# Optimization experiments

Measured on AMD Instinct MI355X. Metric: run time of the kernel, lower is better.

The kernel has to match this reference:

```python
import jax, jax.numpy as jnp
import numpy as np

N = 50000
E = 800000
IN = 256
HID = 64
HEADS = 4
EPS = 1e-5


def batchnorm(x, g, b):
    # training-mode BatchNorm1d over node dim, biased variance (torch semantics)
    mu = jnp.mean(x, axis=0)
    var = jnp.mean((x - mu) ** 2, axis=0)
    return (x - mu) * jax.lax.rsqrt(var + EPS) * g + b


def gat(x, edge_index, W, a_src, a_dst, bias, heads, out_ch, num_nodes):
    src, dst = edge_index[0], edge_index[1]
    h = (x @ W).reshape(num_nodes, heads, out_ch)          # [N,H,C]
    al_s = jnp.einsum('nhc,hc->nh', h, a_src)              # [N,H]
    al_d = jnp.einsum('nhc,hc->nh', h, a_dst)
    e = jax.nn.leaky_relu(al_s[src] + al_d[dst], 0.2)      # [E,H]
    # segment softmax over destination neighborhoods
    m = jax.ops.segment_max(e, dst, num_segments=num_nodes)
    m = jnp.where(jnp.isfinite(m), m, 0.0)
    ex = jnp.exp(e - m[dst])                               # [E,H]
    denom = jax.ops.segment_sum(ex, dst, num_segments=num_nodes)
    alpha = ex / (denom[dst] + 1e-16)                      # [E,H]
    msg = alpha[:, :, None] * h[src]                       # [E,H,C]
    out = jax.ops.segment_sum(msg, dst, num_segments=num_nodes)
    return out.reshape(num_nodes, heads * out_ch) + bias


def setup_inputs() -> dict:
    key = jax.random.key(0)
    ks = jax.random.split(key, 12)
    d = {}
    d['x'] = jax.random.normal(ks[0], (N, IN), jnp.float32)
    d['edge_index'] = jax.random.randint(ks[1], (2, E), 0, N, jnp.int32)
    d['bn1_g'] = jnp.ones((IN,), jnp.float32)
    d['bn1_b'] = jnp.zeros((IN,), jnp.float32)
    d['lin1_W'] = jax.random.normal(ks[2], (IN, HID * HEADS), jnp.float32) * (1.0 / np.sqrt(IN))
    d['lin1_b'] = jnp.zeros((HID * HEADS,), jnp.float32)
    d['con1_W'] = jax.random.normal(ks[3], (IN, HID * HEADS), jnp.float32) * (1.0 / np.sqrt(IN))
    d['con1_asrc'] = jax.random.normal(ks[4], (HEADS, HID), jnp.float32) * 0.1
    d['con1_adst'] = jax.random.normal(ks[5], (HEADS, HID), jnp.float32) * 0.1
    d['con1_b'] = jnp.zeros((HID * HEADS,), jnp.float32)
    d['bn3_g'] = jnp.ones((HID * HEADS,), jnp.float32)
    d['bn3_b'] = jnp.zeros((HID * HEADS,), jnp.float32)
    d['lin3_W'] = jax.random.normal(ks[6], (HID * HEADS, 2), jnp.float32) * (1.0 / np.sqrt(HID * HEADS))
    d['lin3_b'] = jnp.zeros((2,), jnp.float32)
    d['con3_W'] = jax.random.normal(ks[7], (HID * HEADS, 2), jnp.float32) * (1.0 / np.sqrt(HID * HEADS))
    d['con3_asrc'] = jax.random.normal(ks[8], (1, 2), jnp.float32) * 0.1
    d['con3_adst'] = jax.random.normal(ks[9], (1, 2), jnp.float32) * 0.1
    d['con3_b'] = jnp.zeros((2,), jnp.float32)
    return d


def reference(x, edge_index, bn1_g, bn1_b, lin1_W, lin1_b, con1_W, con1_asrc, con1_adst, con1_b,
              bn3_g, bn3_b, lin3_W, lin3_b, con3_W, con3_asrc, con3_adst, con3_b):
    x = batchnorm(x, bn1_g, bn1_b)
    x = jax.nn.relu(x @ lin1_W + lin1_b
                    + gat(x, edge_index, con1_W, con1_asrc, con1_adst, con1_b, HEADS, HID, N))
    x = batchnorm(x, bn3_g, bn3_b)
    x = jax.nn.relu(x @ lin3_W + lin3_b
                    + gat(x, edge_index, con3_W, con3_asrc, con3_adst, con3_b, 1, 2, N))
    return x
```

## Files before the change

kernel.cpp:

```cpp
#include <hip/hip_runtime.h>
#include <math.h>

#define NN 50000
#define NE 800000
#define IC 256
#define EPS 1e-5f
#define P8 50176

typedef __attribute__((ext_vector_type(8))) short short8;
typedef __attribute__((ext_vector_type(4))) float f32x4;

enum : int {
  OFF_S1     = 0,
  OFF_S2     = 256,
  OFF_BAR    = 512,
  OFF_C8     = 528,
  ZERO_END   = OFF_C8 + 8 * P8,
  OFF_COFF   = ZERO_END,
  OFF_START  = OFF_COFF + 8 * P8,
  OFF_RANK   = OFF_START + 50004,
  OFF_BSM    = OFF_RANK + 200000,
  OFF_ALS    = OFF_BSM + 1024,
  OFF_ALD    = OFF_ALS + 200000,
  OFF_SRCS   = OFF_ALD + 200000,
  OFF_Y32    = OFF_SRCS + 800000,
  OFF_ND4    = OFF_Y32 + 100000,
  OFF_BFH    = OFF_ND4 + 200000,
  OFF_HBF    = OFF_BFH + 65536,
  OFF_YLBF   = OFF_HBF + 6400000,
  WS_FLOATS  = OFF_YLBF + 6400000
};

__device__ __forceinline__ float lrelu(float s) { return s > 0.f ? s : 0.2f * s; }
__device__ __forceinline__ float b2f(unsigned short u) {
  return __uint_as_float(((unsigned)u) << 16);
}
__device__ __forceinline__ unsigned short f2bf(float f) {
  unsigned u = __float_as_uint(f);
  return (unsigned short)((u + 0x7fffu + ((u >> 16) & 1u)) >> 16);
}
__device__ __forceinline__ unsigned cvtpk(float lo, float hi) {
  unsigned r;
  asm("v_cvt_pk_bf16_f32 %0, %1, %2" : "=v"(r) : "v"(lo), "v"(hi));
  return r;
}

__global__ __launch_bounds__(256) void k_prep(const float* __restrict__ x,
                                              float* __restrict__ S1,
                                              float* __restrict__ S2,
                                              const float* __restrict__ Wlin,
                                              const float* __restrict__ Wcon,
                                              unsigned short* __restrict__ Bfh) {
  int b = blockIdx.x;
  if (b < 1024) {
    int c = threadIdx.x;
    float s1 = 0.f, s2 = 0.f;
    for (int r0 = b * 8; r0 < NN; r0 += 8192) {
#pragma unroll
      for (int u = 0; u < 8; ++u) {
        int r = r0 + u;
        if (r < NN) {
          float v = x[r * IC + c];
          s1 += v;
          s2 = fmaf(v, v, s2);
        }
      }
    }
    atomicAdd(&S1[c], s1);
    atomicAdd(&S2[c], s2);
  } else {
    int id = (b - 1024) * 256 + threadIdx.x;
    int j = id & 7, lane = (id >> 3) & 63, nt = (id >> 9) & 31, ks = id >> 14;
    int k = ks * 32 + ((lane >> 4) << 3) + j;
    int n = nt * 16 + (lane & 15);
    float v = (n < 256) ? Wlin[k * 256 + n] : Wcon[k * 256 + (n - 256)];
    Bfh[id] = f2bf(v);
  }
}

__global__ __launch_bounds__(256) void k_bnstats2(const ushort4* __restrict__ x1q,
                                                  float* __restrict__ S1,
                                                  float* __restrict__ S2) {
  __shared__ float red1[4][256], red2[4][256];
  const int tid = threadIdx.x, wave = tid >> 6, lane = tid & 63;
  float s1a = 0.f, s1b = 0.f, s1c = 0.f, s1d = 0.f;
  float s2a = 0.f, s2b = 0.f, s2c = 0.f, s2d = 0.f;
  for (int r = blockIdx.x * 4 + wave; r < NN; r += gridDim.x * 4) {
    ushort4 v = x1q[r * 64 + lane];
    float f0 = b2f(v.x), f1 = b2f(v.y), f2 = b2f(v.z), f3 = b2f(v.w);
    s1a += f0; s2a = fmaf(f0, f0, s2a);
    s1b += f1; s2b = fmaf(f1, f1, s2b);
    s1c += f2; s2c = fmaf(f2, f2, s2c);
    s1d += f3; s2d = fmaf(f3, f3, s2d);
  }
  red1[wave][lane * 4 + 0] = s1a; red2[wave][lane * 4 + 0] = s2a;
  red1[wave][lane * 4 + 1] = s1b; red2[wave][lane * 4 + 1] = s2b;
  red1[wave][lane * 4 + 2] = s1c; red2[wave][lane * 4 + 2] = s2c;
  red1[wave][lane * 4 + 3] = s1d; red2[wave][lane * 4 + 3] = s2d;
  __syncthreads();
  float a = red1[0][tid] + red1[1][tid] + red1[2][tid] + red1[3][tid];
  float b = red2[0][tid] + red2[1][tid] + red2[2][tid] + red2[3][tid];
  atomicAdd(&S1[tid], a);
  atomicAdd(&S2[tid], b);
}

__global__ __launch_bounds__(256, 4) void k_gemm(const float* __restrict__ x,
                                                 const float* __restrict__ S1,
                                                 const float* __restrict__ S2,
                                                 const float* __restrict__ bng,
                                                 const float* __restrict__ bnb,
                                                 const unsigned short* __restrict__ Bfh,
                                                 unsigned short* __restrict__ ylbf,
                                                 unsigned short* __restrict__ hbf,
                                                 const float* __restrict__ asrc,
                                                 const float* __restrict__ adst,
                                                 float* __restrict__ als,
                                                 float* __restrict__ ald,
                                                 const int* __restrict__ dst,
                                                 int* __restrict__ counts8,
                                                 unsigned char* __restrict__ rank8) {
  const int tid = threadIdx.x;
  const int g = blockIdx.x;
  if (g >= 1568) {
    int hb = g - 1568;
    int e = hb * 256 + tid;
    int copy = hb & 7;
    int old = atomicAdd(&counts8[copy * P8 + dst[e]], 1);
    rank8[e] = (unsigned char)old;
    return;
  }
  const int row_blk = (g >> 4) * 8 + (g & 7);
  const int bn = (g >> 3) & 1;
  if (row_blk >= 782) return;
  const int row0 = row_blk * 64;
  __shared__ unsigned short Ah[2048];
  __shared__ float sc[256], sh[256];
  const int wave = tid >> 6, lane = tid & 63;
  {
    float mu = S1[tid] * (1.f / NN);
    float var = S2[tid] * (1.f / NN) - mu * mu;
    float ss = bng[tid] / sqrtf(var + EPS);
    sc[tid] = ss;
    sh[tid] = bnb[tid] - mu * ss;
  }
  const float4* x4 = (const float4*)x;
  const short8* Bh8 = (const short8*)Bfh;
  f32x4 acc[4][4];
#pragma unroll
  for (int i = 0; i < 4; ++i)
#pragma unroll
    for (int j = 0; j < 4; ++j) acc[i][j] = (f32x4){0.f, 0.f, 0.f, 0.f};

  const int m = tid >> 2, kg = tid & 3;
  const int r = row0 + m;
  const int aaddr = (((m >> 4) * 64) + ((m & 15) | (kg << 4))) * 8;
  __syncthreads();

  for (int ks = 0; ks < 8; ++ks) {
    const int c0 = ks * 32 + kg * 8;
    float v[8];
    if (r < NN) {
      int base = (r * IC + c0) >> 2;
      float4 fa = x4[base], fb = x4[base + 1];
      v[0] = fa.x; v[1] = fa.y; v[2] = fa.z; v[3] = fa.w;
      v[4] = fb.x; v[5] = fb.y; v[6] = fb.z; v[7] = fb.w;
#pragma unroll
      for (int j = 0; j < 8; ++j) v[j] = fmaf(v[j], sc[c0 + j], sh[c0 + j]);
    } else {
#pragma unroll
      for (int j = 0; j < 8; ++j) v[j] = 0.f;
    }
    unsigned ph[4];
#pragma unroll
    for (int j = 0; j < 4; ++j) ph[j] = cvtpk(v[2 * j], v[2 * j + 1]);
    *(uint4*)&Ah[aaddr] = make_uint4(ph[0], ph[1], ph[2], ph[3]);
    __syncthreads();

    short8 ah[4];
#pragma unroll
    for (int mt = 0; mt < 4; ++mt)
      ah[mt] = *(const short8*)&Ah[(mt * 64 + lane) * 8];
#pragma unroll
    for (int nt = 0; nt < 4; ++nt) {
      short8 bh = Bh8[(ks * 32 + bn * 16 + wave * 4 + nt) * 64 + lane];
#pragma unroll
      for (int mt = 0; mt < 4; ++mt)
        acc[mt][nt] = __builtin_amdgcn_mfma_f32_16x16x32_bf16(ah[mt], bh, acc[mt][nt], 0, 0, 0);
    }
    __syncthreads();
  }
  const int colq = lane & 15, quad = lane >> 4;
  if (bn == 0) {
#pragma unroll
    for (int mt = 0; mt < 4; ++mt)
#pragma unroll
      for (int reg = 0; reg < 4; ++reg) {
        int rr = row0 + mt * 16 + quad * 4 + reg;
        if (rr < NN) {
#pragma unroll
          for (int nt = 0; nt < 4; ++nt)
            ylbf[rr * IC + wave * 64 + nt * 16 + colq] = f2bf(acc[mt][nt][reg]);
        }
      }
  } else {
    const int head = wave;
    float asv[4], adv[4];
#pragma unroll
    for (int j = 0; j < 4; ++j) {
      asv[j] = asrc[head * 64 + j * 16 + colq];
      adv[j] = adst[head * 64 + j * 16 + colq];
    }
#pragma unroll
    for (int mt = 0; mt < 4; ++mt)
#pragma unroll
      for (int reg = 0; reg < 4; ++reg) {
        int rr = row0 + mt * 16 + quad * 4 + reg;
        float sA = 0.f, dA = 0.f;
#pragma unroll
        for (int j = 0; j < 4; ++j) {
          float hA = acc[mt][j][reg];
          sA = fmaf(hA, asv[j], sA);
          dA = fmaf(hA, adv[j], dA);
          if (rr < NN) hbf[rr * IC + head * 64 + j * 16 + colq] = f2bf(hA);
        }
#pragma unroll
        for (int off = 1; off < 16; off <<= 1) {
          sA += __shfl_xor(sA, off, 64);
          dA += __shfl_xor(dA, off, 64);
        }
        if (rr < NN) {
          if (colq == 0) als[rr * 4 + head] = sA;
          else if (colq == 1) ald[rr * 4 + head] = dA;
        }
      }
  }
}

__global__ __launch_bounds__(1024) void k_scan(const int* __restrict__ counts8,
                                               int* __restrict__ coff,
                                               int* __restrict__ start,
                                               float* __restrict__ S1,
                                               float* __restrict__ S2) {
  __shared__ int red[16];
  __shared__ int buf[1024];
  const int tid = threadIdx.x, b = blockIdx.x;
  const int base = b * 1024;
  int pre = 0;
  for (int i = tid; i < base; i += 1024) {
    int s = 0;
#pragma unroll
    for (int k = 0; k < 8; ++k) s += counts8[k * P8 + i];
    pre += s;
  }
#pragma unroll
  for (int off = 1; off < 64; off <<= 1) pre += __shfl_xor(pre, off, 64);
  if ((tid & 63) == 0) red[tid >> 6] = pre;
  if (b == 0 && tid < 256) {
    S1[tid] = 0.f;
    S2[tid] = 0.f;
  }
  __syncthreads();
  int bpre = 0;
#pragma unroll
  for (int w = 0; w < 16; ++w) bpre += red[w];
  const int i = base + tid;
  int pc[8];
  int tot = 0;
#pragma unroll
  for (int k = 0; k < 8; ++k) {
    pc[k] = counts8[k * P8 + i];
    tot += pc[k];
  }
  buf[tid] = tot;
  __syncthreads();
  for (int off = 1; off < 1024; off <<= 1) {
    int t = (tid >= off) ? buf[tid - off] : 0;
    __syncthreads();
    buf[tid] += t;
    __syncthreads();
  }
  int ex = bpre + buf[tid] - tot;
  int run = ex;
#pragma unroll
  for (int k = 0; k < 8; ++k) {
    coff[k * P8 + i] = run;
    run += pc[k];
  }
  if (i < NN) start[i] = ex;
  if (b == 48 && tid == 1023) start[NN] = ex + tot;
}

__global__ __launch_bounds__(256) void k_scatter(const int* __restrict__ src,
                                                 const int* __restrict__ dst,
                                                 const int* __restrict__ coff,
                                                 const unsigned char* __restrict__ rank8,
                                                 int* __restrict__ srcs) {
  int e = blockIdx.x * 256 + threadIdx.x;
  int copy = blockIdx.x & 7;
  int pos = coff[copy * P8 + dst[e]] + (int)rank8[e];
  srcs[pos] = src[e];
}

__global__ __launch_bounds__(256) void k_agg(const ushort4* __restrict__ hq,
                                             ushort4* __restrict__ x1,
                                             const float4* __restrict__ als4,
                                             const float4* __restrict__ ald4,
                                             const int* __restrict__ start,
                                             const int* __restrict__ srcs,
                                             const float4* __restrict__ lb4,
                                             const float4* __restrict__ cb4) {
  __shared__ float lsp[1024];
  const int tid = threadIdx.x;
  const int wave = tid >> 6, lane = tid & 63, head = lane >> 4;
  const int n = blockIdx.x * 4 + wave;
  const float* als = (const float*)als4;
  const int s = start[n], t = start[n + 1];
  const int deg = t - s;
  const float4 aldv = ald4[n];
  int svk = -1;
  float p0 = 0.f, p1 = 0.f, p2 = 0.f, p3 = 0.f;
  if (lane < deg) {
    svk = srcs[s + lane];
    float4 a = als4[svk];
    p0 = __expf(lrelu(a.x + aldv.x));
    p1 = __expf(lrelu(a.y + aldv.y));
    p2 = __expf(lrelu(a.z + aldv.z));
    p3 = __expf(lrelu(a.w + aldv.w));
  }
  *(float4*)&lsp[wave * 256 + lane * 4] = make_float4(p0, p1, p2, p3);
  float d0 = p0, d1 = p1, d2 = p2, d3 = p3;
  const float aldh = head == 0 ? aldv.x : head == 1 ? aldv.y : head == 2 ? aldv.z : aldv.w;
  if (deg > 64) {
    for (int i = s + 64 + lane; i < t; i += 64) {
      float4 a = als4[srcs[i]];
      d0 += __expf(lrelu(a.x + aldv.x));
      d1 += __expf(lrelu(a.y + aldv.y));
      d2 += __expf(lrelu(a.z + aldv.z));
      d3 += __expf(lrelu(a.w + aldv.w));
    }
  }
#pragma unroll
  for (int off = 1; off < 64; off <<= 1) {
    d0 += __shfl_xor(d0, off, 64);
    d1 += __shfl_xor(d1, off, 64);
    d2 += __shfl_xor(d2, off, 64);
    d3 += __shfl_xor(d3, off, 64);
  }
  const float inv =
      1.f / ((head == 0 ? d0 : head == 1 ? d1 : head == 2 ? d2 : d3) + 1e-16f);
  float a0 = 0.f, a1 = 0.f, a2 = 0.f, a3 = 0.f;
  const int cnt = min(deg, 64);
  const int wbase = wave * 256 + head;
  int j = 0;
  for (; j + 4 <= cnt; j += 4) {
    int sv0 = __shfl(svk, j, 64), sv1 = __shfl(svk, j + 1, 64);
    int sv2 = __shfl(svk, j + 2, 64), sv3 = __shfl(svk, j + 3, 64);
    ushort4 hv0 = hq[sv0 * 64 + lane];
    ushort4 hv1 = hq[sv1 * 64 + lane];
    ushort4 hv2 = hq[sv2 * 64 + lane];
    ushort4 hv3 = hq[sv3 * 64 + lane];
    float w0 = lsp[wbase + j * 4], w1 = lsp[wbase + j * 4 + 4];
    float w2 = lsp[wbase + j * 4 + 8], w3 = lsp[wbase + j * 4 + 12];
    a0 = fmaf(w0, b2f(hv0.x), a0); a1 = fmaf(w0, b2f(hv0.y), a1);
    a2 = fmaf(w0, b2f(hv0.z), a2); a3 = fmaf(w0, b2f(hv0.w), a3);
    a0 = fmaf(w1, b2f(hv1.x), a0); a1 = fmaf(w1, b2f(hv1.y), a1);
    a2 = fmaf(w1, b2f(hv1.z), a2); a3 = fmaf(w1, b2f(hv1.w), a3);
    a0 = fmaf(w2, b2f(hv2.x), a0); a1 = fmaf(w2, b2f(hv2.y), a1);
    a2 = fmaf(w2, b2f(hv2.z), a2); a3 = fmaf(w2, b2f(hv2.w), a3);
    a0 = fmaf(w3, b2f(hv3.x), a0); a1 = fmaf(w3, b2f(hv3.y), a1);
    a2 = fmaf(w3, b2f(hv3.z), a2); a3 = fmaf(w3, b2f(hv3.w), a3);
  }
  for (; j < cnt; ++j) {
    int sv = __shfl(svk, j, 64);
    float w = lsp[wbase + j * 4];
    ushort4 hv = hq[sv * 64 + lane];
    a0 = fmaf(w, b2f(hv.x), a0);
    a1 = fmaf(w, b2f(hv.y), a1);
    a2 = fmaf(w, b2f(hv.z), a2);
    a3 = fmaf(w, b2f(hv.w), a3);
  }
  if (deg > 64) {
    for (int i = s + 64; i < t; ++i) {
      int sv = srcs[i];
      float av = als[sv * 4 + head];
      float p = __expf(lrelu(av + aldh));
      ushort4 hv = hq[sv * 64 + lane];
      a0 = fmaf(p, b2f(hv.x), a0);
      a1 = fmaf(p, b2f(hv.y), a1);
      a2 = fmaf(p, b2f(hv.z), a2);
      a3 = fmaf(p, b2f(hv.w), a3);
    }
  }
  ushort4 yb = x1[n * 64 + lane];
  float4 bb1 = lb4[lane], bb2 = cb4[lane];
  ushort4 rb;
  rb.x = f2bf(fmaxf(fmaf(a0, inv, b2f(yb.x) + bb1.x + bb2.x), 0.f));
  rb.y = f2bf(fmaxf(fmaf(a1, inv, b2f(yb.y) + bb1.y + bb2.y), 0.f));
  rb.z = f2bf(fmaxf(fmaf(a2, inv, b2f(yb.z) + bb1.z + bb2.z), 0.f));
  rb.w = f2bf(fmaxf(fmaf(a3, inv, b2f(yb.w) + bb1.w + bb2.w), 0.f));
  x1[n * 64 + lane] = rb;
}

__global__ __launch_bounds__(256) void k_node2(const ushort4* __restrict__ x1,
                                               const float* __restrict__ S1,
                                               const float* __restrict__ S2,
                                               const float* __restrict__ g3,
                                               const float* __restrict__ b3,
                                               const float4* __restrict__ Wl4,
                                               const float4* __restrict__ Wc4,
                                               const float* __restrict__ a3s,
                                               const float* __restrict__ a3d,
                                               const float* __restrict__ l3b,
                                               const float* __restrict__ c3b,
                                               float2* __restrict__ y32,
                                               float4* __restrict__ nd4) {
  __shared__ float sc[256], sh[256];
  const int tid = threadIdx.x;
  {
    float mu = S1[tid] * (1.f / NN);
    float var = S2[tid] * (1.f / NN) - mu * mu;
    float ss = g3[tid] / sqrtf(var + EPS);
    sc[tid] = ss;
    sh[tid] = b3[tid] - mu * ss;
  }
  __syncthreads();
  const int n = blockIdx.x * 4 + (tid >> 6);
  const int lane = tid & 63;
  ushort4 xb = x1[n * 64 + lane];
  float x0 = fmaf(b2f(xb.x), sc[lane * 4 + 0], sh[lane * 4 + 0]);
  float x1v = fmaf(b2f(xb.y), sc[lane * 4 + 1], sh[lane * 4 + 1]);
  float x2 = fmaf(b2f(xb.z), sc[lane * 4 + 2], sh[lane * 4 + 2]);
  float x3 = fmaf(b2f(xb.w), sc[lane * 4 + 3], sh[lane * 4 + 3]);
  float4 wa = Wl4[lane * 2], wb = Wl4[lane * 2 + 1];
  float y0 = x0 * wa.x + x1v * wa.z + x2 * wb.x + x3 * wb.z;
  float y1 = x0 * wa.y + x1v * wa.w + x2 * wb.y + x3 * wb.w;
  float4 ca = Wc4[lane * 2], cb = Wc4[lane * 2 + 1];
  float g0 = x0 * ca.x + x1v * ca.z + x2 * cb.x + x3 * cb.z;
  float g1 = x0 * ca.y + x1v * ca.w + x2 * cb.y + x3 * cb.w;
#pragma unroll
  for (int off = 1; off < 64; off <<= 1) {
    y0 += __shfl_xor(y0, off, 64);
    y1 += __shfl_xor(y1, off, 64);
    g0 += __shfl_xor(g0, off, 64);
    g1 += __shfl_xor(g1, off, 64);
  }
  if (lane == 0) {
    y32[n] = make_float2(y0 + l3b[0] + c3b[0], y1 + l3b[1] + c3b[1]);
    nd4[n] = make_float4(g0 * a3s[0] + g1 * a3s[1], g0, g1,
                         g0 * a3d[0] + g1 * a3d[1]);
  }
}

__global__ __launch_bounds__(256) void k_final(const int* __restrict__ start,
                                               const int* __restrict__ srcs,
                                               const float4* __restrict__ nd4,
                                               const float2* __restrict__ y32,
                                               float* __restrict__ out) {
  const int tid = threadIdx.x;
  const int n = blockIdx.x * 16 + (tid >> 4);
  const int li = tid & 15;
  const int s = start[n], t = start[n + 1];
  const float ad = nd4[n].w;
  float den = 0.f, a0 = 0.f, a1 = 0.f;
  for (int ii = s + li; ii < t; ii += 16) {
    float4 vv = nd4[srcs[ii]];
    float p = __expf(lrelu(vv.x + ad));
    den += p;
    a0 = fmaf(p, vv.y, a0);
    a1 = fmaf(p, vv.z, a1);
  }
#pragma unroll
  for (int off = 1; off < 16; off <<= 1) {
    den += __shfl_xor(den, off, 64);
    a0 += __shfl_xor(a0, off, 64);
    a1 += __shfl_xor(a1, off, 64);
  }
  if (li == 0) {
    float2 y = y32[n];
    float inv = 1.f / (den + 1e-16f);
    out[2 * n] = fmaxf(fmaf(a0, inv, y.x), 0.f);
    out[2 * n + 1] = fmaxf(fmaf(a1, inv, y.y), 0.f);
  }
}

extern "C" void kernel_launch(void* const* d_in, const int* in_sizes, int n_in,
                              void* d_out, int out_size, void* d_ws, size_t ws_size,
                              hipStream_t stream) {
  const float* x = (const float*)d_in[0];
  const int* ei = (const int*)d_in[1];
  const float* bn1_g = (const float*)d_in[2];
  const float* bn1_b = (const float*)d_in[3];
  const float* lin1_W = (const float*)d_in[4];
  const float* lin1_b = (const float*)d_in[5];
  const float* con1_W = (const float*)d_in[6];
  const float* con1_as = (const float*)d_in[7];
  const float* con1_ad = (const float*)d_in[8];
  const float* con1_b = (const float*)d_in[9];
  const float* bn3_g = (const float*)d_in[10];
  const float* bn3_b = (const float*)d_in[11];
  const float* lin3_W = (const float*)d_in[12];
  const float* lin3_b = (const float*)d_in[13];
  const float* con3_W = (const float*)d_in[14];
  const float* con3_as = (const float*)d_in[15];
  const float* con3_ad = (const float*)d_in[16];
  const float* con3_b = (const float*)d_in[17];
  float* ws = (float*)d_ws;
  const int* srcA = ei;
  const int* dstA = ei + NE;

  float* S1 = ws + OFF_S1;
  float* S2 = ws + OFF_S2;
  int* counts8 = (int*)(ws + OFF_C8);
  int* coff = (int*)(ws + OFF_COFF);
  int* start = (int*)(ws + OFF_START);
  unsigned char* rank8 = (unsigned char*)(ws + OFF_RANK);
  float* als = ws + OFF_ALS;
  float* ald = ws + OFF_ALD;
  int* srcs = (int*)(ws + OFF_SRCS);
  float2* y32 = (float2*)(ws + OFF_Y32);
  float4* nd4 = (float4*)(ws + OFF_ND4);
  unsigned short* Bfh = (unsigned short*)(ws + OFF_BFH);
  unsigned short* hbf = (unsigned short*)(ws + OFF_HBF);
  unsigned short* ylbf = (unsigned short*)(ws + OFF_YLBF);

  hipMemsetAsync(ws, 0, (size_t)ZERO_END * sizeof(float), stream);

  k_prep<<<1536, 256, 0, stream>>>(x, S1, S2, lin1_W, con1_W, Bfh);
  k_gemm<<<1568 + 3125, 256, 0, stream>>>(x, S1, S2, bn1_g, bn1_b, Bfh, ylbf,
                                          hbf, con1_as, con1_ad, als, ald, dstA,
                                          counts8, rank8);
  k_scan<<<49, 1024, 0, stream>>>(counts8, coff, start, S1, S2);
  k_scatter<<<3125, 256, 0, stream>>>(srcA, dstA, coff, rank8, srcs);
  k_agg<<<12500, 256, 0, stream>>>((const ushort4*)hbf, (ushort4*)ylbf,
                                   (const float4*)als, (const float4*)ald, start,
                                   srcs, (const float4*)lin1_b,
                                   (const float4*)con1_b);
  k_bnstats2<<<512, 256, 0, stream>>>((const ushort4*)ylbf, S1, S2);
  k_node2<<<12500, 256, 0, stream>>>((const ushort4*)ylbf, S1, S2, bn3_g, bn3_b,
                                     (const float4*)lin3_W, (const float4*)con3_W,
                                     con3_as, con3_ad, lin3_b, con3_b, y32, nd4);
  k_final<<<3125, 256, 0, stream>>>(start, srcs, nd4, y32, (float*)d_out);
}
```

Baseline: 380.5 us.

## Split aggregation gather into two source-index halves and put histogram blocks first

The aggregation loop now makes two passes over each neighbor list, gathering only sources in [0,25000) and then in [25000,50000). The aim is to shrink the working set of the h gather so it fits in cache. The fused GEMM kernel also reorders its grid so the edge-histogram atomic blocks dispatch before the GEMM blocks, with the histogram grid padded to a multiple of 8 so the GEMM block swizzle stays aligned. The cost is a second pass over the shuffled indices and divergent branches per edge, and the cache benefit is only partial because waves run the halves out of sync with each other.

```diff
diff --git a/kernel.cpp b/kernel.cpp
--- a/kernel.cpp
+++ b/kernel.cpp
@@ -6,6 +6,7 @@
 #define IC 256
 #define EPS 1e-5f
 #define P8 50176
+#define HGRID 3128
 
 typedef __attribute__((ext_vector_type(8))) short short8;
 typedef __attribute__((ext_vector_type(4))) float f32x4;
@@ -120,15 +121,16 @@
                                                  int* __restrict__ counts8,
                                                  unsigned char* __restrict__ rank8) {
   const int tid = threadIdx.x;
-  const int g = blockIdx.x;
-  if (g >= 1568) {
-    int hb = g - 1568;
-    int e = hb * 256 + tid;
-    int copy = hb & 7;
+  const int b = blockIdx.x;
+  if (b < HGRID) {
+    if (b >= 3125) return;
+    int e = b * 256 + tid;
+    int copy = b & 7;
     int old = atomicAdd(&counts8[copy * P8 + dst[e]], 1);
     rank8[e] = (unsigned char)old;
     return;
   }
+  const int g = b - HGRID;
   const int row_blk = (g >> 4) * 8 + (g & 7);
   const int bn = (g >> 3) & 1;
   if (row_blk >= 782) return;
@@ -351,44 +353,63 @@
   float a0 = 0.f, a1 = 0.f, a2 = 0.f, a3 = 0.f;
   const int cnt = min(deg, 64);
   const int wbase = wave * 256 + head;
-  int j = 0;
-  for (; j + 4 <= cnt; j += 4) {
-    int sv0 = __shfl(svk, j, 64), sv1 = __shfl(svk, j + 1, 64);
-    int sv2 = __shfl(svk, j + 2, 64), sv3 = __shfl(svk, j + 3, 64);
-    ushort4 hv0 = hq[sv0 * 64 + lane];
-    ushort4 hv1 = hq[sv1 * 64 + lane];
-    ushort4 hv2 = hq[sv2 * 64 + lane];
-    ushort4 hv3 = hq[sv3 * 64 + lane];
-    float w0 = lsp[wbase + j * 4], w1 = lsp[wbase + j * 4 + 4];
-    float w2 = lsp[wbase + j * 4 + 8], w3 = lsp[wbase + j * 4 + 12];
-    a0 = fmaf(w0, b2f(hv0.x), a0); a1 = fmaf(w0, b2f(hv0.y), a1);
-    a2 = fmaf(w0, b2f(hv0.z), a2); a3 = fmaf(w0, b2f(hv0.w), a3);
-    a0 = fmaf(w1, b2f(hv1.x), a0); a1 = fmaf(w1, b2f(hv1.y), a1);
-    a2 = fmaf(w1, b2f(hv1.z), a2); a3 = fmaf(w1, b2f(hv1.w), a3);
-    a0 = fmaf(w2, b2f(hv2.x), a0); a1 = fmaf(w2, b2f(hv2.y), a1);
-    a2 = fmaf(w2, b2f(hv2.z), a2); a3 = fmaf(w2, b2f(hv2.w), a3);
-    a0 = fmaf(w3, b2f(hv3.x), a0); a1 = fmaf(w3, b2f(hv3.y), a1);
-    a2 = fmaf(w3, b2f(hv3.z), a2); a3 = fmaf(w3, b2f(hv3.w), a3);
-  }
-  for (; j < cnt; ++j) {
-    int sv = __shfl(svk, j, 64);
-    float w = lsp[wbase + j * 4];
-    ushort4 hv = hq[sv * 64 + lane];
-    a0 = fmaf(w, b2f(hv.x), a0);
-    a1 = fmaf(w, b2f(hv.y), a1);
-    a2 = fmaf(w, b2f(hv.z), a2);
-    a3 = fmaf(w, b2f(hv.w), a3);
-  }
-  if (deg > 64) {
-    for (int i = s + 64; i < t; ++i) {
-      int sv = srcs[i];
-      float av = als[sv * 4 + head];
-      float p = __expf(lrelu(av + aldh));
-      ushort4 hv = hq[sv * 64 + lane];
-      a0 = fmaf(p, b2f(hv.x), a0);
-      a1 = fmaf(p, b2f(hv.y), a1);
-      a2 = fmaf(p, b2f(hv.z), a2);
-      a3 = fmaf(p, b2f(hv.w), a3);
+#pragma unroll
+  for (int half = 0; half < 2; ++half) {
+    const int lo = half * 25000;
+    const int hi = lo + 25000;
+    int j = 0;
+    for (; j + 4 <= cnt; j += 4) {
+      int sv0 = __shfl(svk, j, 64), sv1 = __shfl(svk, j + 1, 64);
+      int sv2 = __shfl(svk, j + 2, 64), sv3 = __shfl(svk, j + 3, 64);
+      if (sv0 >= lo && sv0 < hi) {
+        float w = lsp[wbase + j * 4];
+        ushort4 hv = hq[sv0 * 64 + lane];
+        a0 = fmaf(w, b2f(hv.x), a0); a1 = fmaf(w, b2f(hv.y), a1);
+        a2 = fmaf(w, b2f(hv.z), a2); a3 = fmaf(w, b2f(hv.w), a3);
+      }
+      if (sv1 >= lo && sv1 < hi) {
+        float w = lsp[wbase + j * 4 + 4];
+        ushort4 hv = hq[sv1 * 64 + lane];
+        a0 = fmaf(w, b2f(hv.x), a0); a1 = fmaf(w, b2f(hv.y), a1);
+        a2 = fmaf(w, b2f(hv.z), a2); a3 = fmaf(w, b2f(hv.w), a3);
+      }
+      if (sv2 >= lo && sv2 < hi) {
+        float w = lsp[wbase + j * 4 + 8];
+        ushort4 hv = hq[sv2 * 64 + lane];
+        a0 = fmaf(w, b2f(hv.x), a0); a1 = fmaf(w, b2f(hv.y), a1);
+        a2 = fmaf(w, b2f(hv.z), a2); a3 = fmaf(w, b2f(hv.w), a3);
+      }
+      if (sv3 >= lo && sv3 < hi) {
+        float w = lsp[wbase + j * 4 + 12];
+        ushort4 hv = hq[sv3 * 64 + lane];
+        a0 = fmaf(w, b2f(hv.x), a0); a1 = fmaf(w, b2f(hv.y), a1);
+        a2 = fmaf(w, b2f(hv.z), a2); a3 = fmaf(w, b2f(hv.w), a3);
+      }
+    }
+    for (; j < cnt; ++j) {
+      int sv = __shfl(svk, j, 64);
+      if (sv >= lo && sv < hi) {
+        float w = lsp[wbase + j * 4];
+        ushort4 hv = hq[sv * 64 + lane];
+        a0 = fmaf(w, b2f(hv.x), a0);
+        a1 = fmaf(w, b2f(hv.y), a1);
+        a2 = fmaf(w, b2f(hv.z), a2);
+        a3 = fmaf(w, b2f(hv.w), a3);
+      }
+    }
+    if (deg > 64) {
+      for (int i = s + 64; i < t; ++i) {
+        int sv = srcs[i];
+        if (sv >= lo && sv < hi) {
+          float av = als[sv * 4 + head];
+          float p = __expf(lrelu(av + aldh));
+          ushort4 hv = hq[sv * 64 + lane];
+          a0 = fmaf(p, b2f(hv.x), a0);
+          a1 = fmaf(p, b2f(hv.y), a1);
+          a2 = fmaf(p, b2f(hv.z), a2);
+          a3 = fmaf(p, b2f(hv.w), a3);
+        }
+      }
     }
   }
   ushort4 yb = x1[n * 64 + lane];
@@ -526,9 +547,9 @@
   hipMemsetAsync(ws, 0, (size_t)ZERO_END * sizeof(float), stream);
 
   k_prep<<<1536, 256, 0, stream>>>(x, S1, S2, lin1_W, con1_W, Bfh);
-  k_gemm<<<1568 + 3125, 256, 0, stream>>>(x, S1, S2, bn1_g, bn1_b, Bfh, ylbf,
-                                          hbf, con1_as, con1_ad, als, ald, dstA,
-                                          counts8, rank8);
+  k_gemm<<<HGRID + 1568, 256, 0, stream>>>(x, S1, S2, bn1_g, bn1_b, Bfh, ylbf,
+                                           hbf, con1_as, con1_ad, als, ald,
+                                           dstA, counts8, rank8);
   k_scan<<<49, 1024, 0, stream>>>(counts8, coff, start, S1, S2);
   k_scatter<<<3125, 256, 0, stream>>>(srcA, dstA, coff, rank8, srcs);
   k_agg<<<12500, 256, 0, stream>>>((const ushort4*)hbf, (ushort4*)ylbf,
```

Result: slower. 393.8 us (+3.5%).

## Fuse layer-2 BatchNorm statistics into aggregation and stage GEMM stores through LDS

Applied to the files above, without the earlier changes.

Accumulates per-column sum and sum-of-squares of the aggregated activations inside k_agg, using block-level LDS reduction and atomics spread over 8 replicated accumulators. This removes the separate k_bnstats2 kernel and its extra read of the activation buffer. GEMM epilogue outputs are staged in shared memory so global stores become coalesced 16-byte row writes instead of scattered 2-byte stores. The cost is many more global atomics and extra LDS use plus barriers in the GEMM.

```diff
diff --git a/kernel.cpp b/kernel.cpp
--- a/kernel.cpp
+++ b/kernel.cpp
@@ -14,7 +14,8 @@
   OFF_S1     = 0,
   OFF_S2     = 256,
   OFF_BAR    = 512,
-  OFF_C8     = 528,
+  OFF_S32    = 528,
+  OFF_C8     = OFF_S32 + 4096,
   ZERO_END   = OFF_C8 + 8 * P8,
   OFF_COFF   = ZERO_END,
   OFF_START  = OFF_COFF + 8 * P8,
@@ -76,32 +77,6 @@
     float v = (n < 256) ? Wlin[k * 256 + n] : Wcon[k * 256 + (n - 256)];
     Bfh[id] = f2bf(v);
   }
-}
-
-__global__ __launch_bounds__(256) void k_bnstats2(const ushort4* __restrict__ x1q,
-                                                  float* __restrict__ S1,
-                                                  float* __restrict__ S2) {
-  __shared__ float red1[4][256], red2[4][256];
-  const int tid = threadIdx.x, wave = tid >> 6, lane = tid & 63;
-  float s1a = 0.f, s1b = 0.f, s1c = 0.f, s1d = 0.f;
-  float s2a = 0.f, s2b = 0.f, s2c = 0.f, s2d = 0.f;
-  for (int r = blockIdx.x * 4 + wave; r < NN; r += gridDim.x * 4) {
-    ushort4 v = x1q[r * 64 + lane];
-    float f0 = b2f(v.x), f1 = b2f(v.y), f2 = b2f(v.z), f3 = b2f(v.w);
-    s1a += f0; s2a = fmaf(f0, f0, s2a);
-    s1b += f1; s2b = fmaf(f1, f1, s2b);
-    s1c += f2; s2c = fmaf(f2, f2, s2c);
-    s1d += f3; s2d = fmaf(f3, f3, s2d);
-  }
-  red1[wave][lane * 4 + 0] = s1a; red2[wave][lane * 4 + 0] = s2a;
-  red1[wave][lane * 4 + 1] = s1b; red2[wave][lane * 4 + 1] = s2b;
-  red1[wave][lane * 4 + 2] = s1c; red2[wave][lane * 4 + 2] = s2c;
-  red1[wave][lane * 4 + 3] = s1d; red2[wave][lane * 4 + 3] = s2d;
-  __syncthreads();
-  float a = red1[0][tid] + red1[1][tid] + red1[2][tid] + red1[3][tid];
-  float b = red2[0][tid] + red2[1][tid] + red2[2][tid] + red2[3][tid];
-  atomicAdd(&S1[tid], a);
-  atomicAdd(&S2[tid], b);
 }
 
 __global__ __launch_bounds__(256, 4) void k_gemm(const float* __restrict__ x,
@@ -135,6 +110,7 @@
   const int row0 = row_blk * 64;
   __shared__ unsigned short Ah[2048];
   __shared__ float sc[256], sh[256];
+  __shared__ unsigned short Cst[32 * 256];
   const int wave = tid >> 6, lane = tid & 63;
   {
     float mu = S1[tid] * (1.f / NN);
@@ -192,16 +168,29 @@
   const int colq = lane & 15, quad = lane >> 4;
   if (bn == 0) {
 #pragma unroll
-    for (int mt = 0; mt < 4; ++mt)
-#pragma unroll
-      for (int reg = 0; reg < 4; ++reg) {
-        int rr = row0 + mt * 16 + quad * 4 + reg;
-        if (rr < NN) {
+    for (int half = 0; half < 2; ++half) {
+#pragma unroll
+      for (int mh = 0; mh < 2; ++mh) {
+        const int mt = half * 2 + mh;
+#pragma unroll
+        for (int reg = 0; reg < 4; ++reg)
 #pragma unroll
           for (int nt = 0; nt < 4; ++nt)
-            ylbf[rr * IC + wave * 64 + nt * 16 + colq] = f2bf(acc[mt][nt][reg]);
-        }
+            Cst[(mh * 16 + quad * 4 + reg) * 256 + wave * 64 + nt * 16 + colq] =
+                f2bf(acc[mt][nt][reg]);
       }
+      __syncthreads();
+#pragma unroll
+      for (int c = 0; c < 4; ++c) {
+        int chunk = c * 256 + tid;
+        int row = chunk >> 5;
+        int col8 = (chunk & 31) * 8;
+        int rr = row0 + half * 32 + row;
+        if (rr < NN)
+          *(uint4*)&ylbf[rr * IC + col8] = *(const uint4*)&Cst[row * 256 + col8];
+      }
+      __syncthreads();
+    }
   } else {
     const int head = wave;
     float asv[4], adv[4];
@@ -211,36 +200,51 @@
       adv[j] = adst[head * 64 + j * 16 + colq];
     }
 #pragma unroll
-    for (int mt = 0; mt < 4; ++mt)
-#pragma unroll
-      for (int reg = 0; reg < 4; ++reg) {
-        int rr = row0 + mt * 16 + quad * 4 + reg;
-        float sA = 0.f, dA = 0.f;
-#pragma unroll
-        for (int j = 0; j < 4; ++j) {
-          float hA = acc[mt][j][reg];
-          sA = fmaf(hA, asv[j], sA);
-          dA = fmaf(hA, adv[j], dA);
-          if (rr < NN) hbf[rr * IC + head * 64 + j * 16 + colq] = f2bf(hA);
-        }
-#pragma unroll
-        for (int off = 1; off < 16; off <<= 1) {
-          sA += __shfl_xor(sA, off, 64);
-          dA += __shfl_xor(dA, off, 64);
-        }
-        if (rr < NN) {
-          if (colq == 0) als[rr * 4 + head] = sA;
-          else if (colq == 1) ald[rr * 4 + head] = dA;
+    for (int half = 0; half < 2; ++half) {
+#pragma unroll
+      for (int mh = 0; mh < 2; ++mh) {
+        const int mt = half * 2 + mh;
+#pragma unroll
+        for (int reg = 0; reg < 4; ++reg) {
+          int rr = row0 + mt * 16 + quad * 4 + reg;
+          float sA = 0.f, dA = 0.f;
+#pragma unroll
+          for (int j = 0; j < 4; ++j) {
+            float hA = acc[mt][j][reg];
+            sA = fmaf(hA, asv[j], sA);
+            dA = fmaf(hA, adv[j], dA);
+            Cst[(mh * 16 + quad * 4 + reg) * 256 + head * 64 + j * 16 + colq] =
+                f2bf(hA);
+          }
+#pragma unroll
+          for (int off = 1; off < 16; off <<= 1) {
+            sA += __shfl_xor(sA, off, 64);
+            dA += __shfl_xor(dA, off, 64);
+          }
+          if (rr < NN) {
+            if (colq == 0) als[rr * 4 + head] = sA;
+            else if (colq == 1) ald[rr * 4 + head] = dA;
+          }
         }
       }
+      __syncthreads();
+#pragma unroll
+      for (int c = 0; c < 4; ++c) {
+        int chunk = c * 256 + tid;
+        int row = chunk >> 5;
+        int col8 = (chunk & 31) * 8;
+        int rr = row0 + half * 32 + row;
+        if (rr < NN)
+          *(uint4*)&hbf[rr * IC + col8] = *(const uint4*)&Cst[row * 256 + col8];
+      }
+      __syncthreads();
+    }
   }
 }
 
 __global__ __launch_bounds__(1024) void k_scan(const int* __restrict__ counts8,
                                                int* __restrict__ coff,
-                                               int* __restrict__ start,
-                                               float* __restrict__ S1,
-                                               float* __restrict__ S2) {
+                                               int* __restrict__ start) {
   __shared__ int red[16];
   __shared__ int buf[1024];
   const int tid = threadIdx.x, b = blockIdx.x;
@@ -255,10 +259,6 @@
 #pragma unroll
   for (int off = 1; off < 64; off <<= 1) pre += __shfl_xor(pre, off, 64);
   if ((tid & 63) == 0) red[tid >> 6] = pre;
-  if (b == 0 && tid < 256) {
-    S1[tid] = 0.f;
-    S2[tid] = 0.f;
-  }
   __syncthreads();
   int bpre = 0;
 #pragma unroll
@@ -308,8 +308,9 @@
                                              const int* __restrict__ start,
                                              const int* __restrict__ srcs,
                                              const float4* __restrict__ lb4,
-                                             const float4* __restrict__ cb4) {
-  __shared__ float lsp[1024];
+                                             const float4* __restrict__ cb4,
+                                             float* __restrict__ S32) {
+  __shared__ float lsp[2048];
   const int tid = threadIdx.x;
   const int wave = tid >> 6, lane = tid & 63, head = lane >> 4;
   const int n = blockIdx.x * 4 + wave;
@@ -399,11 +400,22 @@
   rb.z = f2bf(fmaxf(fmaf(a2, inv, b2f(yb.z) + bb1.z + bb2.z), 0.f));
   rb.w = f2bf(fmaxf(fmaf(a3, inv, b2f(yb.w) + bb1.w + bb2.w), 0.f));
   x1[n * 64 + lane] = rb;
+  {
+    float f0 = b2f(rb.x), f1 = b2f(rb.y), f2 = b2f(rb.z), f3 = b2f(rb.w);
+    *(float4*)&lsp[wave * 256 + lane * 4] = make_float4(f0, f1, f2, f3);
+    *(float4*)&lsp[1024 + wave * 256 + lane * 4] =
+        make_float4(f0 * f0, f1 * f1, f2 * f2, f3 * f3);
+  }
+  __syncthreads();
+  float sa = lsp[tid] + lsp[256 + tid] + lsp[512 + tid] + lsp[768 + tid];
+  float sb = lsp[1024 + tid] + lsp[1280 + tid] + lsp[1536 + tid] + lsp[1792 + tid];
+  const int copy = blockIdx.x & 7;
+  atomicAdd(&S32[copy * 512 + tid], sa);
+  atomicAdd(&S32[copy * 512 + 256 + tid], sb);
 }
 
 __global__ __launch_bounds__(256) void k_node2(const ushort4* __restrict__ x1,
-                                               const float* __restrict__ S1,
-                                               const float* __restrict__ S2,
+                                               const float* __restrict__ S32,
                                                const float* __restrict__ g3,
                                                const float* __restrict__ b3,
                                                const float4* __restrict__ Wl4,
@@ -417,8 +429,14 @@
   __shared__ float sc[256], sh[256];
   const int tid = threadIdx.x;
   {
-    float mu = S1[tid] * (1.f / NN);
-    float var = S2[tid] * (1.f / NN) - mu * mu;
+    float s1 = 0.f, s2 = 0.f;
+#pragma unroll
+    for (int c = 0; c < 8; ++c) {
+      s1 += S32[c * 512 + tid];
+      s2 += S32[c * 512 + 256 + tid];
+    }
+    float mu = s1 * (1.f / NN);
+    float var = s2 * (1.f / NN) - mu * mu;
     float ss = g3[tid] / sqrtf(var + EPS);
     sc[tid] = ss;
     sh[tid] = b3[tid] - mu * ss;
@@ -510,6 +528,7 @@
 
   float* S1 = ws + OFF_S1;
   float* S2 = ws + OFF_S2;
+  float* S32 = ws + OFF_S32;
   int* counts8 = (int*)(ws + OFF_C8);
   int* coff = (int*)(ws + OFF_COFF);
   int* start = (int*)(ws + OFF_START);
@@ -529,14 +548,13 @@
   k_gemm<<<1568 + 3125, 256, 0, stream>>>(x, S1, S2, bn1_g, bn1_b, Bfh, ylbf,
                                           hbf, con1_as, con1_ad, als, ald, dstA,
                                           counts8, rank8);
-  k_scan<<<49, 1024, 0, stream>>>(counts8, coff, start, S1, S2);
+  k_scan<<<49, 1024, 0, stream>>>(counts8, coff, start);
   k_scatter<<<3125, 256, 0, stream>>>(srcA, dstA, coff, rank8, srcs);
   k_agg<<<12500, 256, 0, stream>>>((const ushort4*)hbf, (ushort4*)ylbf,
                                    (const float4*)als, (const float4*)ald, start,
                                    srcs, (const float4*)lin1_b,
-                                   (const float4*)con1_b);
-  k_bnstats2<<<512, 256, 0, stream>>>((const ushort4*)ylbf, S1, S2);
-  k_node2<<<12500, 256, 0, stream>>>((const ushort4*)ylbf, S1, S2, bn3_g, bn3_b,
+                                   (const float4*)con1_b, S32);
+  k_node2<<<12500, 256, 0, stream>>>((const ushort4*)ylbf, S32, bn3_g, bn3_b,
                                      (const float4*)lin3_W, (const float4*)con3_W,
                                      con3_as, con3_ad, lin3_b, con3_b, y32, nd4);
   k_final<<<3125, 256, 0, stream>>>(start, srcs, nd4, y32, (float*)d_out);
```

Measured after the change: 371.0 us. 1.03x faster.
